# Optimization experiments

Measured on AMD Instinct MI355X. Metric: run time of the kernel, lower is better.

## Reference

```python
import jax, jax.numpy as jnp
import numpy as np


def setup_inputs() -> dict:
    key = jax.random.key(0)
    k1, k2, k3 = jax.random.split(key, 3)
    B, N, D, T = 8, 2, 256, 500
    SPK = 2000
    H = jax.random.normal(k1, (B, N, D, T), dtype=jnp.float32)
    S = jax.random.randint(k2, (B, N, T), 0, SPK, dtype=jnp.int64)
    E = jax.random.normal(k3, (SPK, D), dtype=jnp.float32)
    alpha = jnp.ones((1,), dtype=jnp.float32) * 10.0
    beta = jnp.ones((1,), dtype=jnp.float32) * 5.0
    return {"H": H, "S": S, "E": E, "alpha": alpha, "beta": beta, "N": 2}


def reference(H, S, E, alpha, beta, N):
    # H: (B, N, D, T); S: (B, N, T) int ids; E: (SPK, D)
    B, N_, D, T = H.shape
    # embedding lookup: (B, N, T, D) -> (B, N, D, T)
    E_S = jnp.transpose(E[S], (0, 1, 3, 2))
    # pairwise dist between predicted vectors and active-speaker embeddings
    # (B, N_pred=N, N_emb=N, T) -- small, direct broadcast
    Dist_p = jnp.sum((H[:, None, :, :, :] - E_S[:, :, None, :, :]) ** 2, axis=3)
    # N == 2 path matching (identity vs swap), min over the two alignments
    p0 = Dist_p[:, 0, 0, :] + Dist_p[:, 1, 1, :]  # (B, T)
    p1 = Dist_p[:, 0, 1, :] + Dist_p[:, 1, 0, :]  # (B, T)
    Dmin = jnp.minimum(p0, p1)                    # (B, T)
    Dmin = -alpha * Dmin + beta                   # broadcast (1,) over (B, T)
    # full distance to every speaker: ||H||^2 + ||E||^2 - 2 H.E
    # avoids materializing (B, SPK, N, D, T)
    Hsq = jnp.sum(H * H, axis=2)                  # (B, N, T)
    Esq = jnp.sum(E * E, axis=1)                  # (SPK,)
    cross = jnp.einsum('bndt,sd->bsnt', H, E)     # (B, SPK, N, T)
    Dist = Hsq[:, None, :, :] + Esq[None, :, None, None] - 2.0 * cross
    Dist = -alpha * Dist + beta                   # (B, SPK, N, T)
    lse = jax.nn.logsumexp(Dist, axis=1)          # (B, N, T)
    loss = -jnp.mean(Dmin) + jnp.mean(lse)
    return (E_S[:, :, :, 0], loss)
```

## Files before the change

kernel.cpp:

```cpp
#include <hip/hip_runtime.h>
#include <math.h>

#define Bb   8
#define Dd   256
#define Tt   500
#define SPK  2000
#define SPKP 2048
#define BN   16
#define L2E  1.4426950408889634f
#define LN2  0.6931471805599453f

#define EXP2F(x) __builtin_amdgcn_exp2f(x)
#define LOG2F(x) __builtin_amdgcn_logf(x)

#define F_ESN   0
#define F_DMINP 2048
#define F_HSQP  4096
#define F_PM    36864
#define F_PL    69632
#define EBF_BYTES ((size_t)102400 * 4)
#define HBF_BYTES (EBF_BYTES + (size_t)1048576)

typedef __bf16 v8bf __attribute__((ext_vector_type(8)));
typedef float  v4f  __attribute__((ext_vector_type(4)));

__device__ inline unsigned pack_bf16x2(float lo, float hi) {
    union { __bf16 h; unsigned short u; } a, b;
    a.h = (__bf16)lo; b.h = (__bf16)hi;
    return ((unsigned)b.u << 16) | (unsigned)a.u;
}

__global__ __launch_bounds__(256) void prep_all_kernel(
        const float* __restrict__ E, const int* __restrict__ S,
        const float* __restrict__ H, const float* __restrict__ alpha,
        const float* __restrict__ beta, float* __restrict__ ws,
        float* __restrict__ out) {
    int bid = blockIdx.x;
    int tid = threadIdx.x;

    if (bid < 512) {
        int s = bid * 4 + (tid >> 6);
        int lane = tid & 63;
        float4 v = make_float4(0.f, 0.f, 0.f, 0.f);
        if (s < SPK) v = ((const float4*)E)[s * 64 + lane];
        __bf16* ebf = (__bf16*)((char*)ws + EBF_BYTES);
        uint2 pp;
        pp.x = pack_bf16x2(v.x, v.y);
        pp.y = pack_bf16x2(v.z, v.w);
        *(uint2*)(ebf + (size_t)s * Dd + lane * 4) = pp;
        float acc = v.x * v.x + v.y * v.y + v.z * v.z + v.w * v.w;
        #pragma unroll
        for (int off = 32; off > 0; off >>= 1) acc += __shfl_down(acc, off, 64);
        if (lane == 0) ws[F_ESN + s] = (s < SPK) ? (-alpha[0] * acc * L2E) : -1e30f;
    } else if (bid < 528) {
        int i = (bid - 512) * 256 + tid;
        int bn = i >> 8, d = i & 255;
        out[i] = E[(size_t)S[bn * Tt] * Dd + d];
    } else if (bid < 656) {
        __shared__ float4 shm[8][32];
        int qq = bid - 528;
        int b = qq >> 4;
        int t0 = (qq & 15) * 32;
        int tl = tid & 31;
        int wv = tid >> 5;
        int t = t0 + tl;
        bool ok = (t < Tt);
        int tc = ok ? t : (Tt - 1);
        int s0 = S[(b * 2 + 0) * Tt + tc];
        int s1 = S[(b * 2 + 1) * Tt + tc];
        const float* h0 = H + ((size_t)(b * 2 + 0) * Dd) * Tt + tc;
        const float* h1 = H + ((size_t)(b * 2 + 1) * Dd) * Tt + tc;
        const float* e0 = E + (size_t)s0 * Dd;
        const float* e1 = E + (size_t)s1 * Dd;
        float d00 = 0, d01 = 0, d10 = 0, d11 = 0;
        int dbase = wv * 32;
        #pragma unroll 4
        for (int dd = 0; dd < 32; ++dd) {
            int d = dbase + dd;
            float x0 = h0[(size_t)d * Tt], x1 = h1[(size_t)d * Tt];
            float y0 = e0[d], y1 = e1[d];
            float u;
            u = x0 - y0; d00 = fmaf(u, u, d00);
            u = x0 - y1; d01 = fmaf(u, u, d01);
            u = x1 - y0; d10 = fmaf(u, u, d10);
            u = x1 - y1; d11 = fmaf(u, u, d11);
        }
        shm[wv][tl] = make_float4(d00, d01, d10, d11);
        __syncthreads();
        if (tid < 32) {
            d00 = 0; d01 = 0; d10 = 0; d11 = 0;
            #pragma unroll
            for (int g = 0; g < 8; ++g) {
                float4 p = shm[g][tl];
                d00 += p.x; d01 += p.y; d10 += p.z; d11 += p.w;
            }
            float dm = fminf(d00 + d11, d01 + d10);
            float val = ok ? (-alpha[0] * dm + beta[0]) : 0.f;
            #pragma unroll
            for (int off = 16; off > 0; off >>= 1) val += __shfl_down(val, off, 32);
            if (tid == 0) ws[F_DMINP + qq] = val;
        }
    } else {
        __shared__ float trans[32][65];
        int u = bid - 656;
        int bn = u >> 6;
        int r = u & 63;
        int tt0 = (r & 15) * 32;
        int d0 = (r >> 4) * 64;
        const float* Hb = H + (size_t)bn * Dd * Tt;
        #pragma unroll
        for (int p = 0; p < 8; ++p) {
            int flat = p * 256 + tid;
            int dd = flat >> 5;
            int tl = flat & 31;
            int t = tt0 + tl;
            trans[tl][dd] = (t < Tt) ? Hb[(size_t)(d0 + dd) * Tt + t] : 0.f;
        }
        __syncthreads();
        int tw = tid >> 3;
        int j = tid & 7;
        float sq = 0.f;
        float vals[8];
        #pragma unroll
        for (int e = 0; e < 8; ++e) {
            float x = trans[tw][j * 8 + e];
            vals[e] = x;
            sq = fmaf(x, x, sq);
        }
        sq += __shfl_xor(sq, 1, 64);
        sq += __shfl_xor(sq, 2, 64);
        sq += __shfl_xor(sq, 4, 64);
        uint4 pk;
        pk.x = pack_bf16x2(vals[0], vals[1]);
        pk.y = pack_bf16x2(vals[2], vals[3]);
        pk.z = pack_bf16x2(vals[4], vals[5]);
        pk.w = pack_bf16x2(vals[6], vals[7]);
        __bf16* hbf = (__bf16*)((char*)ws + HBF_BYTES);
        *(uint4*)(hbf + ((size_t)(bn * 512 + tt0 + tw) * Dd + d0 + j * 8)) = pk;
        if (j == 0) ws[F_HSQP + (size_t)(bn * 512 + tt0 + tw) * 4 + (r >> 4)] = sq;
    }
}

__global__ __launch_bounds__(256, 2) void lse_mfma_kernel(
        const float* __restrict__ alpha, const float* __restrict__ beta,
        float* __restrict__ ws) {
    __shared__ __bf16 shB[64 * 264];
    __shared__ __bf16 shA[64 * 264];
    __shared__ float mrg_m[4][4][16], mrg_l[4][4][16];

    int bn = blockIdx.x;
    int t0 = blockIdx.y * 64;
    int mz = blockIdx.z;
    int tid = threadIdx.x;
    int lane = tid & 63;
    int n = lane & 15;
    int q = lane >> 4;
    int w = tid >> 6;

    const __bf16* ebf = (const __bf16*)((const char*)ws + EBF_BYTES);
    const __bf16* hbf = (const __bf16*)((const char*)ws + HBF_BYTES);

    #pragma unroll
    for (int p = 0; p < 8; ++p) {
        int flat = p * 256 + tid;
        int row = flat >> 5;
        int ch = flat & 31;
        uint4 v = *(const uint4*)(hbf + ((size_t)(bn * 512 + t0 + row) * Dd + ch * 8));
        *(uint4*)(shB + row * 264 + ch * 8) = v;
    }
    __syncthreads();

    v8bf bq[4][8];
    #pragma unroll
    for (int i = 0; i < 4; ++i) {
        int tloc = 16 * i + n;
        #pragma unroll
        for (int ks = 0; ks < 8; ++ks) {
            bq[i][ks] = *reinterpret_cast<const v8bf*>(&shB[tloc * 264 + ks * 32 + q * 8]);
        }
    }

    float A = alpha[0], Bv = beta[0];
    float ta2p = 2.f * A * L2E;
    float ctc2[4];
    #pragma unroll
    for (int i = 0; i < 4; ++i) {
        int t = t0 + 16 * i + n;
        float4 hq = *(const float4*)(ws + F_HSQP + (size_t)(bn * 512 + t) * 4);
        float hs = hq.x + hq.y + hq.z + hq.w;
        ctc2[i] = (t < Tt) ? ((Bv - A * hs) * L2E) : 0.f;
    }

    float lm[4], ll[4];
    #pragma unroll
    for (int i = 0; i < 4; ++i) { lm[i] = -INFINITY; ll[i] = 0.f; }

    for (int c = 0; c < 8; ++c) {
        int sbase = mz * 512 + c * 64;
        __syncthreads();
        #pragma unroll
        for (int p = 0; p < 8; ++p) {
            int flat = p * 256 + tid;
            int row = flat >> 5;
            int ch = flat & 31;
            uint4 v = *(const uint4*)(ebf + ((size_t)(sbase + row) * Dd + ch * 8));
            *(uint4*)(shA + row * 264 + ch * 8) = v;
        }
        __syncthreads();

        int sb = sbase + w * 16;
        v8bf af[8];
        #pragma unroll
        for (int ks = 0; ks < 8; ++ks) {
            af[ks] = *reinterpret_cast<const v8bf*>(&shA[(w * 16 + n) * 264 + ks * 32 + q * 8]);
        }
        float4 es4 = *(const float4*)(ws + F_ESN + sb + q * 4);

        v4f acc[4];
        #pragma unroll
        for (int i = 0; i < 4; ++i) acc[i] = (v4f){0.f, 0.f, 0.f, 0.f};
        #pragma unroll
        for (int ks = 0; ks < 8; ++ks) {
            #pragma unroll
            for (int i = 0; i < 4; ++i) {
                acc[i] = __builtin_amdgcn_mfma_f32_16x16x32_bf16(af[ks], bq[i][ks], acc[i], 0, 0, 0);
            }
        }
        float e0 = es4.x, e1 = es4.y, e2 = es4.z, e3 = es4.w;
        #pragma unroll
        for (int i = 0; i < 4; ++i) {
            float c2 = ctc2[i];
            float v0 = fmaf(ta2p, acc[i][0], c2 + e0);
            float v1 = fmaf(ta2p, acc[i][1], c2 + e1);
            float v2 = fmaf(ta2p, acc[i][2], c2 + e2);
            float v3 = fmaf(ta2p, acc[i][3], c2 + e3);
            float vm = fmaxf(fmaxf(v0, v1), fmaxf(v2, v3));
            float s = EXP2F(v0 - vm) + EXP2F(v1 - vm) + EXP2F(v2 - vm) + EXP2F(v3 - vm);
            float nm = fmaxf(lm[i], vm);
            ll[i] = ll[i] * EXP2F(lm[i] - nm) + s * EXP2F(vm - nm);
            lm[i] = nm;
        }
    }

    #pragma unroll
    for (int i = 0; i < 4; ++i) {
        float m = lm[i], l = ll[i];
        #pragma unroll
        for (int msk = 16; msk <= 32; msk <<= 1) {
            float om = __shfl_xor(m, msk, 64);
            float ol = __shfl_xor(l, msk, 64);
            float nm = fmaxf(m, om);
            l = l * EXP2F(m - nm) + ol * EXP2F(om - nm);
            m = nm;
        }
        if (q == 0) { mrg_m[w][i][n] = m; mrg_l[w][i][n] = l; }
    }
    __syncthreads();

    if (tid < 64) {
        int i = tid >> 4, cc = tid & 15;
        float m = mrg_m[0][i][cc], l = mrg_l[0][i][cc];
        #pragma unroll
        for (int wv = 1; wv < 4; ++wv) {
            float om = mrg_m[wv][i][cc], ol = mrg_l[wv][i][cc];
            float nm = fmaxf(m, om);
            l = l * EXP2F(m - nm) + ol * EXP2F(om - nm);
            m = nm;
        }
        int tw = t0 + 16 * i + cc;
        if (tw < Tt) {
            ws[F_PM + (bn * 512 + tw) * 4 + mz] = m;
            ws[F_PL + (bn * 512 + tw) * 4 + mz] = l;
        }
    }
}

__global__ __launch_bounds__(1024) void final_kernel(const float* __restrict__ ws,
                                                     float* __restrict__ out) {
    __shared__ float rL[16], rD[16];
    int tid = threadIdx.x;
    float lsum = 0.f;
    #pragma unroll
    for (int it = 0; it < 8; ++it) {
        int idx = it * 1024 + tid;
        int bn = idx >> 9, t = idx & 511;
        if (t < Tt) {
            int base = (bn * 512 + t) * 4;
            float m = ws[F_PM + base], l = ws[F_PL + base];
            #pragma unroll
            for (int s = 1; s < 4; ++s) {
                float om = ws[F_PM + base + s], ol = ws[F_PL + base + s];
                float nm = fmaxf(m, om);
                l = l * EXP2F(m - nm) + ol * EXP2F(om - nm);
                m = nm;
            }
            lsum += LN2 * (m + LOG2F(l));
        }
    }
    float dsum = (tid < 128) ? ws[F_DMINP + tid] : 0.f;
    #pragma unroll
    for (int off = 32; off > 0; off >>= 1) {
        lsum += __shfl_down(lsum, off, 64);
        dsum += __shfl_down(dsum, off, 64);
    }
    if ((tid & 63) == 0) { rL[tid >> 6] = lsum; rD[tid >> 6] = dsum; }
    __syncthreads();
    if (tid == 0) {
        float L = 0.f, D = 0.f;
        #pragma unroll
        for (int wv = 0; wv < 16; ++wv) { L += rL[wv]; D += rD[wv]; }
        out[BN * Dd] = -(D / (float)(Bb * Tt)) + L / (float)(BN * Tt);
    }
}

extern "C" void kernel_launch(void* const* d_in, const int* in_sizes, int n_in,
                              void* d_out, int out_size, void* d_ws, size_t ws_size,
                              hipStream_t stream) {
    const float* H     = (const float*)d_in[0];
    const int*   S     = (const int*)d_in[1];
    const float* E     = (const float*)d_in[2];
    const float* alpha = (const float*)d_in[3];
    const float* beta  = (const float*)d_in[4];
    float* out = (float*)d_out;
    float* ws  = (float*)d_ws;

    prep_all_kernel<<<1680, 256, 0, stream>>>(E, S, H, alpha, beta, ws, out);
    lse_mfma_kernel<<<dim3(BN, 8, 4), 256, 0, stream>>>(alpha, beta, ws);
    final_kernel<<<1, 1024, 0, stream>>>(ws, out);
}
```

Measured before the change: 100.6 us.

## Fuse final reduction into LSE kernel via atomic last-block completion

Removes the separate final reduction kernel. The LSE blocks now count completions per time tile with atomics, and the last block for each tile merges the partial logsumexp values and adds them to a global accumulator. The Dmin and embedding-output work moves from the prep kernel into spare blocks of the LSE launch, which cuts the launch count from three to two. This adds atomic and fence overhead, and the result depends on counters that are reset inside the prep kernel. A dead lse_fused_kernel with placeholder code was also left in.

```diff
diff --git a/kernel.cpp b/kernel.cpp
--- a/kernel.cpp
+++ b/kernel.cpp
@@ -14,7 +14,10 @@
 #define LOG2F(x) __builtin_amdgcn_logf(x)
 
 #define F_ESN   0
-#define F_DMINP 2048
+#define F_CNT   2176
+#define F_DONE  2304
+#define F_LACC  2305
+#define F_DACC  2306
 #define F_HSQP  4096
 #define F_PM    36864
 #define F_PL    69632
@@ -30,15 +33,14 @@
     return ((unsigned)b.u << 16) | (unsigned)a.u;
 }
 
-__global__ __launch_bounds__(256) void prep_all_kernel(
-        const float* __restrict__ E, const int* __restrict__ S,
-        const float* __restrict__ H, const float* __restrict__ alpha,
-        const float* __restrict__ beta, float* __restrict__ ws,
-        float* __restrict__ out) {
+__global__ __launch_bounds__(256) void prep_kernel(
+        const float* __restrict__ E, const float* __restrict__ H,
+        const float* __restrict__ alpha, float* __restrict__ ws) {
     int bid = blockIdx.x;
     int tid = threadIdx.x;
 
     if (bid < 512) {
+        if (bid == 0 && tid < 132) ws[F_CNT + tid] = 0.f;
         int s = bid * 4 + (tid >> 6);
         int lane = tid & 63;
         float4 v = make_float4(0.f, 0.f, 0.f, 0.f);
@@ -52,13 +54,436 @@
         #pragma unroll
         for (int off = 32; off > 0; off >>= 1) acc += __shfl_down(acc, off, 64);
         if (lane == 0) ws[F_ESN + s] = (s < SPK) ? (-alpha[0] * acc * L2E) : -1e30f;
-    } else if (bid < 528) {
-        int i = (bid - 512) * 256 + tid;
+    } else {
+        __shared__ float trans[32][65];
+        int u = bid - 512;
+        int bn = u >> 6;
+        int r = u & 63;
+        int tt0 = (r & 15) * 32;
+        int d0 = (r >> 4) * 64;
+        const float* Hb = H + (size_t)bn * Dd * Tt;
+        #pragma unroll
+        for (int p = 0; p < 8; ++p) {
+            int flat = p * 256 + tid;
+            int dd = flat >> 5;
+            int tl = flat & 31;
+            int t = tt0 + tl;
+            trans[tl][dd] = (t < Tt) ? Hb[(size_t)(d0 + dd) * Tt + t] : 0.f;
+        }
+        __syncthreads();
+        int tw = tid >> 3;
+        int j = tid & 7;
+        float sq = 0.f;
+        float vals[8];
+        #pragma unroll
+        for (int e = 0; e < 8; ++e) {
+            float x = trans[tw][j * 8 + e];
+            vals[e] = x;
+            sq = fmaf(x, x, sq);
+        }
+        sq += __shfl_xor(sq, 1, 64);
+        sq += __shfl_xor(sq, 2, 64);
+        sq += __shfl_xor(sq, 4, 64);
+        uint4 pk;
+        pk.x = pack_bf16x2(vals[0], vals[1]);
+        pk.y = pack_bf16x2(vals[2], vals[3]);
+        pk.z = pack_bf16x2(vals[4], vals[5]);
+        pk.w = pack_bf16x2(vals[6], vals[7]);
+        __bf16* hbf = (__bf16*)((char*)ws + HBF_BYTES);
+        *(uint4*)(hbf + ((size_t)(bn * 512 + tt0 + tw) * Dd + d0 + j * 8)) = pk;
+        if (j == 0) ws[F_HSQP + (size_t)(bn * 512 + tt0 + tw) * 4 + (r >> 4)] = sq;
+    }
+}
+
+__global__ __launch_bounds__(256, 2) void lse_fused_kernel(
+        const float* __restrict__ E, const int* __restrict__ S,
+        const float* __restrict__ alpha, const float* __restrict__ beta,
+        float* __restrict__ ws, float* __restrict__ out) {
+    __shared__ __align__(16) unsigned char smem[69632];
+    int bid = blockIdx.x;
+    int tid = threadIdx.x;
+
+    if (bid < 512) {
+        __bf16* shB = (__bf16*)smem;
+        __bf16* shA = (__bf16*)(smem + 33792);
+        float* mrgm = (float*)(smem + 67584);
+        float* mrgl = (float*)(smem + 68608);
+
+        int bn = bid >> 5;
+        int rr = bid & 31;
+        int tt = rr >> 2;
+        int mz = rr & 3;
+        int t0 = tt * 64;
+        int lane = tid & 63;
+        int n = lane & 15;
+        int q = lane >> 4;
+        int w = tid >> 6;
+
+        const __bf16* ebf = (const __bf16*)((const char*)ws + EBF_BYTES);
+        const __bf16* hbf = (const __bf16*)((const char*)ws + HBF_BYTES);
+
+        #pragma unroll
+        for (int p = 0; p < 8; ++p) {
+            int flat = p * 256 + tid;
+            int row = flat >> 5;
+            int ch = flat & 31;
+            uint4 v = *(const uint4*)(hbf + ((size_t)(bn * 512 + t0 + row) * Dd + ch * 8));
+            *(uint4*)(shB + row * 264 + ch * 8) = v;
+        }
+        __syncthreads();
+
+        v8bf bq[4][8];
+        #pragma unroll
+        for (int i = 0; i < 4; ++i) {
+            int tloc = 16 * i + n;
+            #pragma unroll
+            for (int ks = 0; ks < 8; ++ks) {
+                bq[i][ks] = *reinterpret_cast<const v8bf*>(&shB[tloc * 264 + ks * 32 + q * 8]);
+            }
+        }
+
+        float A = alpha[0], Bv = beta[0];
+        float ta2p = 2.f * A * L2E;
+        float ctc2[4];
+        #pragma unroll
+        for (int i = 0; i < 4; ++i) {
+            int t = t0 + 16 * i + n;
+            float4 hq = *(const float4*)(ws + F_HSQP + (size_t)(bn * 512 + t) * 4);
+            float hs = hq.x + hq.y + hq.z + hq.w;
+            ctc2[i] = (t < Tt) ? ((Bv - A * hs) * L2E) : 0.f;
+        }
+
+        float lm[4], ll[4];
+        #pragma unroll
+        for (int i = 0; i < 4; ++i) { lm[i] = -INFINITY; ll[i] = 0.f; }
+
+        for (int c = 0; c < 8; ++c) {
+            int sbase = mz * 512 + c * 64;
+            __syncthreads();
+            #pragma unroll
+            for (int p = 0; p < 8; ++p) {
+                int flat = p * 256 + tid;
+                int row = flat >> 5;
+                int ch = flat & 31;
+                uint4 v = *(const uint4*)(ebf + ((size_t)(sbase + row) * Dd + ch * 8));
+                *(uint4*)(shA + row * 264 + ch * 8) = v;
+            }
+            __syncthreads();
+
+            int sb = sbase + w * 16;
+            v8bf af[8];
+            #pragma unroll
+            for (int ks = 0; ks < 8; ++ks) {
+                af[ks] = *reinterpret_cast<const v8bf*>(&shA[(w * 16 + n) * 264 + ks * 32 + q * 8]);
+            }
+            float4 es4 = *(const float4*)(ws + F_ESN + sb + q * 4);
+
+            v4f acc[4];
+            #pragma unroll
+            for (int i = 0; i < 4; ++i) acc[i] = (v4f){0.f, 0.f, 0.f, 0.f};
+            #pragma unroll
+            for (int ks = 0; ks < 8; ++ks) {
+                #pragma unroll
+                for (int i = 0; i < 4; ++i) {
+                    acc[i] = __builtin_amdgcn_mfma_f32_16x16x32_bf16(af[ks], bq[i][ks], acc[i], 0, 0, 0);
+                }
+            }
+            float e0 = es4.x, e1 = es4.y, e2 = es4.z, e3 = es4.w;
+            #pragma unroll
+            for (int i = 0; i < 4; ++i) {
+                float c2 = ctc2[i];
+                float v0 = fmaf(ta2p, acc[i][0], c2 + e0);
+                float v1 = fmaf(ta2p, acc[i][1], c2 + e1);
+                float v2 = fmaf(ta2p, acc[i][2], c2 + e2);
+                float v3 = fmaf(ta2p, acc[i][3], c2 + e3);
+                float vm = fmaxf(fmaxf(v0, v1), fmaxf(v2, v3));
+                float s = EXP2F(v0 - vm) + EXP2F(v1 - vm) + EXP2F(v2 - vm) + EXP2F(v3 - vm);
+                float nm = fmaxf(lm[i], vm);
+                ll[i] = ll[i] * EXP2F(lm[i] - nm) + s * EXP2F(vm - nm);
+                lm[i] = nm;
+            }
+        }
+
+        #pragma unroll
+        for (int i = 0; i < 4; ++i) {
+            float m = lm[i], l = ll[i];
+            #pragma unroll
+            for (int msk = 16; msk <= 32; msk <<= 1) {
+                float om = __shfl_xor(m, msk, 64);
+                float ol = __shfl_xor(l, msk, 64);
+                float nm = fmaxf(m, om);
+                l = l * EXP2F(m - nm) + ol * EXP2F(om - nm);
+                m = nm;
+            }
+            if (q == 0) { mrgm[(w * 4 + i) * 16 + n] = m; mrgl[(w * 4 + i) * 16 + n] = l; }
+        }
+        __syncthreads();
+
+        if (tid < 64) {
+            int i = tid >> 4, cc = tid & 15;
+            float m = mrgm[i * 16 + cc], l = mrgl[i * 16 + cc];
+            #pragma unroll
+            for (int wv = 1; wv < 4; ++wv) {
+                float om = mrgm[(wv * 4 + i) * 16 + cc], ol = mrgl[(wv * 4 + i) * 16 + cc];
+                float nm = fmaxf(m, om);
+                l = l * EXP2F(m - nm) + ol * EXP2F(om - nm);
+                m = nm;
+            }
+            int tw = t0 + 16 * i + cc;
+            if (tw < Tt) {
+                ws[F_PM + (bn * 512 + tw) * 4 + mz] = m;
+                ws[F_PL + (bn * 512 + tw) * 4 + mz] = l;
+            }
+        }
+        __syncthreads();
+
+        int g = bn * 8 + tt;
+        int* flag = (int*)mrgm;
+        if (tid == 0) {
+            __threadfence();
+            unsigned old = atomicAdd((unsigned*)(ws + F_CNT) + g, 1u);
+            *flag = (old == 3u) ? 1 : 0;
+        }
+        __syncthreads();
+        if (*flag && tid < 64) {
+            __threadfence();
+            float lsum = 0.f;
+            int t = t0 + tid;
+            if (t < Tt) {
+                int base = (bn * 512 + t) * 4;
+                float m = ws[F_PM + base], l = ws[F_PL + base];
+                #pragma unroll
+                for (int s = 1; s < 4; ++s) {
+                    float om = ws[F_PM + base + s], ol = ws[F_PL + base + s];
+                    float nm = fmaxf(m, om);
+                    l = l * EXP2F(m - nm) + ol * EXP2F(om - nm);
+                    m = nm;
+                }
+                lsum = LN2 * (m + LOG2F(l));
+            }
+            #pragma unroll
+            for (int off = 32; off > 0; off >>= 1) lsum += __shfl_down(lsum, off, 64);
+            if (tid == 0) {
+                atomicAdd(ws + F_LACC, lsum);
+                __threadfence();
+                unsigned d = atomicAdd((unsigned*)(ws + F_DONE), 1u);
+                if (d == 255u) {
+                    __threadfence();
+                    float L = atomicAdd(ws + F_LACC, 0.f);
+                    float D = atomicAdd(ws + F_DACC, 0.f);
+                    out[BN * Dd] = -(D / (float)(Bb * Tt)) + L / (float)(BN * Tt);
+                }
+            }
+        }
+    } else if (bid < 640) {
+        float4 (*shm)[32] = (float4(*)[32])smem;
+        int qq = bid - 512;
+        int b = qq >> 4;
+        int t0 = (qq & 15) * 32;
+        int tl = tid & 31;
+        int wv = tid >> 5;
+        int t = t0 + tl;
+        bool ok = (t < Tt);
+        int tc = ok ? t : (Tt - 1);
+        const float* H = E - 0;
+        (void)H;
+        shm[0][0].x = 0.f;
+        extern __device__ int __dummy_never_defined;
+        const float* Hraw = (const float*)S;
+        (void)Hraw;
+        {
+        }
+    } else {
+        int i = (bid - 640) * 256 + tid;
         int bn = i >> 8, d = i & 255;
         out[i] = E[(size_t)S[bn * Tt] * Dd + d];
-    } else if (bid < 656) {
-        __shared__ float4 shm[8][32];
-        int qq = bid - 528;
+    }
+}
+
+__global__ __launch_bounds__(256, 2) void lse_fused2_kernel(
+        const float* __restrict__ E, const int* __restrict__ S,
+        const float* __restrict__ H, const float* __restrict__ alpha,
+        const float* __restrict__ beta, float* __restrict__ ws,
+        float* __restrict__ out) {
+    __shared__ __align__(16) unsigned char smem[69632];
+    int bid = blockIdx.x;
+    int tid = threadIdx.x;
+
+    if (bid < 512) {
+        __bf16* shB = (__bf16*)smem;
+        __bf16* shA = (__bf16*)(smem + 33792);
+        float* mrgm = (float*)(smem + 67584);
+        float* mrgl = (float*)(smem + 68608);
+
+        int bn = bid >> 5;
+        int rr = bid & 31;
+        int tt = rr >> 2;
+        int mz = rr & 3;
+        int t0 = tt * 64;
+        int lane = tid & 63;
+        int n = lane & 15;
+        int q = lane >> 4;
+        int w = tid >> 6;
+
+        const __bf16* ebf = (const __bf16*)((const char*)ws + EBF_BYTES);
+        const __bf16* hbf = (const __bf16*)((const char*)ws + HBF_BYTES);
+
+        #pragma unroll
+        for (int p = 0; p < 8; ++p) {
+            int flat = p * 256 + tid;
+            int row = flat >> 5;
+            int ch = flat & 31;
+            uint4 v = *(const uint4*)(hbf + ((size_t)(bn * 512 + t0 + row) * Dd + ch * 8));
+            *(uint4*)(shB + row * 264 + ch * 8) = v;
+        }
+        __syncthreads();
+
+        v8bf bq[4][8];
+        #pragma unroll
+        for (int i = 0; i < 4; ++i) {
+            int tloc = 16 * i + n;
+            #pragma unroll
+            for (int ks = 0; ks < 8; ++ks) {
+                bq[i][ks] = *reinterpret_cast<const v8bf*>(&shB[tloc * 264 + ks * 32 + q * 8]);
+            }
+        }
+
+        float A = alpha[0], Bv = beta[0];
+        float ta2p = 2.f * A * L2E;
+        float ctc2[4];
+        #pragma unroll
+        for (int i = 0; i < 4; ++i) {
+            int t = t0 + 16 * i + n;
+            float4 hq = *(const float4*)(ws + F_HSQP + (size_t)(bn * 512 + t) * 4);
+            float hs = hq.x + hq.y + hq.z + hq.w;
+            ctc2[i] = (t < Tt) ? ((Bv - A * hs) * L2E) : 0.f;
+        }
+
+        float lm[4], ll[4];
+        #pragma unroll
+        for (int i = 0; i < 4; ++i) { lm[i] = -INFINITY; ll[i] = 0.f; }
+
+        for (int c = 0; c < 8; ++c) {
+            int sbase = mz * 512 + c * 64;
+            __syncthreads();
+            #pragma unroll
+            for (int p = 0; p < 8; ++p) {
+                int flat = p * 256 + tid;
+                int row = flat >> 5;
+                int ch = flat & 31;
+                uint4 v = *(const uint4*)(ebf + ((size_t)(sbase + row) * Dd + ch * 8));
+                *(uint4*)(shA + row * 264 + ch * 8) = v;
+            }
+            __syncthreads();
+
+            int sb = sbase + w * 16;
+            v8bf af[8];
+            #pragma unroll
+            for (int ks = 0; ks < 8; ++ks) {
+                af[ks] = *reinterpret_cast<const v8bf*>(&shA[(w * 16 + n) * 264 + ks * 32 + q * 8]);
+            }
+            float4 es4 = *(const float4*)(ws + F_ESN + sb + q * 4);
+
+            v4f acc[4];
+            #pragma unroll
+            for (int i = 0; i < 4; ++i) acc[i] = (v4f){0.f, 0.f, 0.f, 0.f};
+            #pragma unroll
+            for (int ks = 0; ks < 8; ++ks) {
+                #pragma unroll
+                for (int i = 0; i < 4; ++i) {
+                    acc[i] = __builtin_amdgcn_mfma_f32_16x16x32_bf16(af[ks], bq[i][ks], acc[i], 0, 0, 0);
+                }
+            }
+            float e0 = es4.x, e1 = es4.y, e2 = es4.z, e3 = es4.w;
+            #pragma unroll
+            for (int i = 0; i < 4; ++i) {
+                float c2 = ctc2[i];
+                float v0 = fmaf(ta2p, acc[i][0], c2 + e0);
+                float v1 = fmaf(ta2p, acc[i][1], c2 + e1);
+                float v2 = fmaf(ta2p, acc[i][2], c2 + e2);
+                float v3 = fmaf(ta2p, acc[i][3], c2 + e3);
+                float vm = fmaxf(fmaxf(v0, v1), fmaxf(v2, v3));
+                float s = EXP2F(v0 - vm) + EXP2F(v1 - vm) + EXP2F(v2 - vm) + EXP2F(v3 - vm);
+                float nm = fmaxf(lm[i], vm);
+                ll[i] = ll[i] * EXP2F(lm[i] - nm) + s * EXP2F(vm - nm);
+                lm[i] = nm;
+            }
+        }
+
+        #pragma unroll
+        for (int i = 0; i < 4; ++i) {
+            float m = lm[i], l = ll[i];
+            #pragma unroll
+            for (int msk = 16; msk <= 32; msk <<= 1) {
+                float om = __shfl_xor(m, msk, 64);
+                float ol = __shfl_xor(l, msk, 64);
+                float nm = fmaxf(m, om);
+                l = l * EXP2F(m - nm) + ol * EXP2F(om - nm);
+                m = nm;
+            }
+            if (q == 0) { mrgm[(w * 4 + i) * 16 + n] = m; mrgl[(w * 4 + i) * 16 + n] = l; }
+        }
+        __syncthreads();
+
+        if (tid < 64) {
+            int i = tid >> 4, cc = tid & 15;
+            float m = mrgm[i * 16 + cc], l = mrgl[i * 16 + cc];
+            #pragma unroll
+            for (int wv = 1; wv < 4; ++wv) {
+                float om = mrgm[(wv * 4 + i) * 16 + cc], ol = mrgl[(wv * 4 + i) * 16 + cc];
+                float nm = fmaxf(m, om);
+                l = l * EXP2F(m - nm) + ol * EXP2F(om - nm);
+                m = nm;
+            }
+            int tw = t0 + 16 * i + cc;
+            if (tw < Tt) {
+                ws[F_PM + (bn * 512 + tw) * 4 + mz] = m;
+                ws[F_PL + (bn * 512 + tw) * 4 + mz] = l;
+            }
+        }
+        __syncthreads();
+
+        int g = bn * 8 + tt;
+        int* flag = (int*)mrgm;
+        if (tid == 0) {
+            __threadfence();
+            unsigned old = atomicAdd((unsigned*)(ws + F_CNT) + g, 1u);
+            *flag = (old == 3u) ? 1 : 0;
+        }
+        __syncthreads();
+        if (*flag && tid < 64) {
+            __threadfence();
+            float lsum = 0.f;
+            int t = t0 + tid;
+            if (t < Tt) {
+                int base = (bn * 512 + t) * 4;
+                float m = ws[F_PM + base], l = ws[F_PL + base];
+                #pragma unroll
+                for (int s = 1; s < 4; ++s) {
+                    float om = ws[F_PM + base + s], ol = ws[F_PL + base + s];
+                    float nm = fmaxf(m, om);
+                    l = l * EXP2F(m - nm) + ol * EXP2F(om - nm);
+                    m = nm;
+                }
+                lsum = LN2 * (m + LOG2F(l));
+            }
+            #pragma unroll
+            for (int off = 32; off > 0; off >>= 1) lsum += __shfl_down(lsum, off, 64);
+            if (tid == 0) {
+                atomicAdd(ws + F_LACC, lsum);
+                __threadfence();
+                unsigned d = atomicAdd((unsigned*)(ws + F_DONE), 1u);
+                if (d == 255u) {
+                    __threadfence();
+                    float L = atomicAdd(ws + F_LACC, 0.f);
+                    float D = atomicAdd(ws + F_DACC, 0.f);
+                    out[BN * Dd] = -(D / (float)(Bb * Tt)) + L / (float)(BN * Tt);
+                }
+            }
+        }
+    } else if (bid < 640) {
+        float4 (*shm)[32] = (float4(*)[32])smem;
+        int qq = bid - 512;
         int b = qq >> 4;
         int t0 = (qq & 15) * 32;
         int tl = tid & 31;
@@ -98,218 +523,22 @@
             float val = ok ? (-alpha[0] * dm + beta[0]) : 0.f;
             #pragma unroll
             for (int off = 16; off > 0; off >>= 1) val += __shfl_down(val, off, 32);
-            if (tid == 0) ws[F_DMINP + qq] = val;
+            if (tid == 0) {
+                atomicAdd(ws + F_DACC, val);
+                __threadfence();
+                unsigned d = atomicAdd((unsigned*)(ws + F_DONE), 1u);
+                if (d == 255u) {
+                    __threadfence();
+                    float L = atomicAdd(ws + F_LACC, 0.f);
+                    float D = atomicAdd(ws + F_DACC, 0.f);
+                    out[BN * Dd] = -(D / (float)(Bb * Tt)) + L / (float)(BN * Tt);
+                }
+            }
         }
     } else {
-        __shared__ float trans[32][65];
-        int u = bid - 656;
-        int bn = u >> 6;
-        int r = u & 63;
-        int tt0 = (r & 15) * 32;
-        int d0 = (r >> 4) * 64;
-        const float* Hb = H + (size_t)bn * Dd * Tt;
-        #pragma unroll
-        for (int p = 0; p < 8; ++p) {
-            int flat = p * 256 + tid;
-            int dd = flat >> 5;
-            int tl = flat & 31;
-            int t = tt0 + tl;
-            trans[tl][dd] = (t < Tt) ? Hb[(size_t)(d0 + dd) * Tt + t] : 0.f;
-        }
-        __syncthreads();
-        int tw = tid >> 3;
-        int j = tid & 7;
-        float sq = 0.f;
-        float vals[8];
-        #pragma unroll
-        for (int e = 0; e < 8; ++e) {
-            float x = trans[tw][j * 8 + e];
-            vals[e] = x;
-            sq = fmaf(x, x, sq);
-        }
-        sq += __shfl_xor(sq, 1, 64);
-        sq += __shfl_xor(sq, 2, 64);
-        sq += __shfl_xor(sq, 4, 64);
-        uint4 pk;
-        pk.x = pack_bf16x2(vals[0], vals[1]);
-        pk.y = pack_bf16x2(vals[2], vals[3]);
-        pk.z = pack_bf16x2(vals[4], vals[5]);
-        pk.w = pack_bf16x2(vals[6], vals[7]);
-        __bf16* hbf = (__bf16*)((char*)ws + HBF_BYTES);
-        *(uint4*)(hbf + ((size_t)(bn * 512 + tt0 + tw) * Dd + d0 + j * 8)) = pk;
-        if (j == 0) ws[F_HSQP + (size_t)(bn * 512 + tt0 + tw) * 4 + (r >> 4)] = sq;
-    }
-}
-
-__global__ __launch_bounds__(256, 2) void lse_mfma_kernel(
-        const float* __restrict__ alpha, const float* __restrict__ beta,
-        float* __restrict__ ws) {
-    __shared__ __bf16 shB[64 * 264];
-    __shared__ __bf16 shA[64 * 264];
-    __shared__ float mrg_m[4][4][16], mrg_l[4][4][16];
-
-    int bn = blockIdx.x;
-    int t0 = blockIdx.y * 64;
-    int mz = blockIdx.z;
-    int tid = threadIdx.x;
-    int lane = tid & 63;
-    int n = lane & 15;
-    int q = lane >> 4;
-    int w = tid >> 6;
-
-    const __bf16* ebf = (const __bf16*)((const char*)ws + EBF_BYTES);
-    const __bf16* hbf = (const __bf16*)((const char*)ws + HBF_BYTES);
-
-    #pragma unroll
-    for (int p = 0; p < 8; ++p) {
-        int flat = p * 256 + tid;
-        int row = flat >> 5;
-        int ch = flat & 31;
-        uint4 v = *(const uint4*)(hbf + ((size_t)(bn * 512 + t0 + row) * Dd + ch * 8));
-        *(uint4*)(shB + row * 264 + ch * 8) = v;
-    }
-    __syncthreads();
-
-    v8bf bq[4][8];
-    #pragma unroll
-    for (int i = 0; i < 4; ++i) {
-        int tloc = 16 * i + n;
-        #pragma unroll
-        for (int ks = 0; ks < 8; ++ks) {
-            bq[i][ks] = *reinterpret_cast<const v8bf*>(&shB[tloc * 264 + ks * 32 + q * 8]);
-        }
-    }
-
-    float A = alpha[0], Bv = beta[0];
-    float ta2p = 2.f * A * L2E;
-    float ctc2[4];
-    #pragma unroll
-    for (int i = 0; i < 4; ++i) {
-        int t = t0 + 16 * i + n;
-        float4 hq = *(const float4*)(ws + F_HSQP + (size_t)(bn * 512 + t) * 4);
-        float hs = hq.x + hq.y + hq.z + hq.w;
-        ctc2[i] = (t < Tt) ? ((Bv - A * hs) * L2E) : 0.f;
-    }
-
-    float lm[4], ll[4];
-    #pragma unroll
-    for (int i = 0; i < 4; ++i) { lm[i] = -INFINITY; ll[i] = 0.f; }
-
-    for (int c = 0; c < 8; ++c) {
-        int sbase = mz * 512 + c * 64;
-        __syncthreads();
-        #pragma unroll
-        for (int p = 0; p < 8; ++p) {
-            int flat = p * 256 + tid;
-            int row = flat >> 5;
-            int ch = flat & 31;
-            uint4 v = *(const uint4*)(ebf + ((size_t)(sbase + row) * Dd + ch * 8));
-            *(uint4*)(shA + row * 264 + ch * 8) = v;
-        }
-        __syncthreads();
-
-        int sb = sbase + w * 16;
-        v8bf af[8];
-        #pragma unroll
-        for (int ks = 0; ks < 8; ++ks) {
-            af[ks] = *reinterpret_cast<const v8bf*>(&shA[(w * 16 + n) * 264 + ks * 32 + q * 8]);
-        }
-        float4 es4 = *(const float4*)(ws + F_ESN + sb + q * 4);
-
-        v4f acc[4];
-        #pragma unroll
-        for (int i = 0; i < 4; ++i) acc[i] = (v4f){0.f, 0.f, 0.f, 0.f};
-        #pragma unroll
-        for (int ks = 0; ks < 8; ++ks) {
-            #pragma unroll
-            for (int i = 0; i < 4; ++i) {
-                acc[i] = __builtin_amdgcn_mfma_f32_16x16x32_bf16(af[ks], bq[i][ks], acc[i], 0, 0, 0);
-            }
-        }
-        float e0 = es4.x, e1 = es4.y, e2 = es4.z, e3 = es4.w;
-        #pragma unroll
-        for (int i = 0; i < 4; ++i) {
-            float c2 = ctc2[i];
-            float v0 = fmaf(ta2p, acc[i][0], c2 + e0);
-            float v1 = fmaf(ta2p, acc[i][1], c2 + e1);
-            float v2 = fmaf(ta2p, acc[i][2], c2 + e2);
-            float v3 = fmaf(ta2p, acc[i][3], c2 + e3);
-            float vm = fmaxf(fmaxf(v0, v1), fmaxf(v2, v3));
-            float s = EXP2F(v0 - vm) + EXP2F(v1 - vm) + EXP2F(v2 - vm) + EXP2F(v3 - vm);
-            float nm = fmaxf(lm[i], vm);
-            ll[i] = ll[i] * EXP2F(lm[i] - nm) + s * EXP2F(vm - nm);
-            lm[i] = nm;
-        }
-    }
-
-    #pragma unroll
-    for (int i = 0; i < 4; ++i) {
-        float m = lm[i], l = ll[i];
-        #pragma unroll
-        for (int msk = 16; msk <= 32; msk <<= 1) {
-            float om = __shfl_xor(m, msk, 64);
-            float ol = __shfl_xor(l, msk, 64);
-            float nm = fmaxf(m, om);
-            l = l * EXP2F(m - nm) + ol * EXP2F(om - nm);
-            m = nm;
-        }
-        if (q == 0) { mrg_m[w][i][n] = m; mrg_l[w][i][n] = l; }
-    }
-    __syncthreads();
-
-    if (tid < 64) {
-        int i = tid >> 4, cc = tid & 15;
-        float m = mrg_m[0][i][cc], l = mrg_l[0][i][cc];
-        #pragma unroll
-        for (int wv = 1; wv < 4; ++wv) {
-            float om = mrg_m[wv][i][cc], ol = mrg_l[wv][i][cc];
-            float nm = fmaxf(m, om);
-            l = l * EXP2F(m - nm) + ol * EXP2F(om - nm);
-            m = nm;
-        }
-        int tw = t0 + 16 * i + cc;
-        if (tw < Tt) {
-            ws[F_PM + (bn * 512 + tw) * 4 + mz] = m;
-            ws[F_PL + (bn * 512 + tw) * 4 + mz] = l;
-        }
-    }
-}
-
-__global__ __launch_bounds__(1024) void final_kernel(const float* __restrict__ ws,
-                                                     float* __restrict__ out) {
-    __shared__ float rL[16], rD[16];
-    int tid = threadIdx.x;
-    float lsum = 0.f;
-    #pragma unroll
-    for (int it = 0; it < 8; ++it) {
-        int idx = it * 1024 + tid;
-        int bn = idx >> 9, t = idx & 511;
-        if (t < Tt) {
-            int base = (bn * 512 + t) * 4;
-            float m = ws[F_PM + base], l = ws[F_PL + base];
-            #pragma unroll
-            for (int s = 1; s < 4; ++s) {
-                float om = ws[F_PM + base + s], ol = ws[F_PL + base + s];
-                float nm = fmaxf(m, om);
-                l = l * EXP2F(m - nm) + ol * EXP2F(om - nm);
-                m = nm;
-            }
-            lsum += LN2 * (m + LOG2F(l));
-        }
-    }
-    float dsum = (tid < 128) ? ws[F_DMINP + tid] : 0.f;
-    #pragma unroll
-    for (int off = 32; off > 0; off >>= 1) {
-        lsum += __shfl_down(lsum, off, 64);
-        dsum += __shfl_down(dsum, off, 64);
-    }
-    if ((tid & 63) == 0) { rL[tid >> 6] = lsum; rD[tid >> 6] = dsum; }
-    __syncthreads();
-    if (tid == 0) {
-        float L = 0.f, D = 0.f;
-        #pragma unroll
-        for (int wv = 0; wv < 16; ++wv) { L += rL[wv]; D += rD[wv]; }
-        out[BN * Dd] = -(D / (float)(Bb * Tt)) + L / (float)(BN * Tt);
+        int i = (bid - 640) * 256 + tid;
+        int bn = i >> 8, d = i & 255;
+        out[i] = E[(size_t)S[bn * Tt] * Dd + d];
     }
 }
 
@@ -324,7 +553,6 @@
     float* out = (float*)d_out;
     float* ws  = (float*)d_ws;
 
-    prep_all_kernel<<<1680, 256, 0, stream>>>(E, S, H, alpha, beta, ws, out);
-    lse_mfma_kernel<<<dim3(BN, 8, 4), 256, 0, stream>>>(alpha, beta, ws);
-    final_kernel<<<1, 1024, 0, stream>>>(ws, out);
+    prep_kernel<<<1536, 256, 0, stream>>>(E, H, alpha, ws);
+    lse_fused2_kernel<<<656, 256, 0, stream>>>(E, S, H, alpha, beta, ws, out);
 }
```

Result: slower. 129.1 us (+28.3%).

## Fuse H transpose, bf16 conversion and norm into the LSE MFMA kernel

Applied to the files above, without the earlier changes.

Removes the prep-stage blocks that transposed H to bf16 in workspace and computed per-row squared norms. Instead, each LSE block reads H directly from global memory, packs it to bf16 in shared memory, and computes the squared norms in place. This drops a workspace write/read round trip and shrinks the prep grid. The cost is that each H tile is now reloaded by the 4 mz blocks, and the loads are strided per d row.

```diff
diff --git a/kernel.cpp b/kernel.cpp
--- a/kernel.cpp
+++ b/kernel.cpp
@@ -15,11 +15,9 @@
 
 #define F_ESN   0
 #define F_DMINP 2048
-#define F_HSQP  4096
-#define F_PM    36864
-#define F_PL    69632
-#define EBF_BYTES ((size_t)102400 * 4)
-#define HBF_BYTES (EBF_BYTES + (size_t)1048576)
+#define F_PM    4096
+#define F_PL    36864
+#define EBF_BYTES ((size_t)69632 * 4)
 
 typedef __bf16 v8bf __attribute__((ext_vector_type(8)));
 typedef float  v4f  __attribute__((ext_vector_type(4)));
@@ -30,7 +28,7 @@
     return ((unsigned)b.u << 16) | (unsigned)a.u;
 }
 
-__global__ __launch_bounds__(256) void prep_all_kernel(
+__global__ __launch_bounds__(256) void prep_kernel(
         const float* __restrict__ E, const int* __restrict__ S,
         const float* __restrict__ H, const float* __restrict__ alpha,
         const float* __restrict__ beta, float* __restrict__ ws,
@@ -56,7 +54,7 @@
         int i = (bid - 512) * 256 + tid;
         int bn = i >> 8, d = i & 255;
         out[i] = E[(size_t)S[bn * Tt] * Dd + d];
-    } else if (bid < 656) {
+    } else {
         __shared__ float4 shm[8][32];
         int qq = bid - 528;
         int b = qq >> 4;
@@ -100,53 +98,16 @@
             for (int off = 16; off > 0; off >>= 1) val += __shfl_down(val, off, 32);
             if (tid == 0) ws[F_DMINP + qq] = val;
         }
-    } else {
-        __shared__ float trans[32][65];
-        int u = bid - 656;
-        int bn = u >> 6;
-        int r = u & 63;
-        int tt0 = (r & 15) * 32;
-        int d0 = (r >> 4) * 64;
-        const float* Hb = H + (size_t)bn * Dd * Tt;
-        #pragma unroll
-        for (int p = 0; p < 8; ++p) {
-            int flat = p * 256 + tid;
-            int dd = flat >> 5;
-            int tl = flat & 31;
-            int t = tt0 + tl;
-            trans[tl][dd] = (t < Tt) ? Hb[(size_t)(d0 + dd) * Tt + t] : 0.f;
-        }
-        __syncthreads();
-        int tw = tid >> 3;
-        int j = tid & 7;
-        float sq = 0.f;
-        float vals[8];
-        #pragma unroll
-        for (int e = 0; e < 8; ++e) {
-            float x = trans[tw][j * 8 + e];
-            vals[e] = x;
-            sq = fmaf(x, x, sq);
-        }
-        sq += __shfl_xor(sq, 1, 64);
-        sq += __shfl_xor(sq, 2, 64);
-        sq += __shfl_xor(sq, 4, 64);
-        uint4 pk;
-        pk.x = pack_bf16x2(vals[0], vals[1]);
-        pk.y = pack_bf16x2(vals[2], vals[3]);
-        pk.z = pack_bf16x2(vals[4], vals[5]);
-        pk.w = pack_bf16x2(vals[6], vals[7]);
-        __bf16* hbf = (__bf16*)((char*)ws + HBF_BYTES);
-        *(uint4*)(hbf + ((size_t)(bn * 512 + tt0 + tw) * Dd + d0 + j * 8)) = pk;
-        if (j == 0) ws[F_HSQP + (size_t)(bn * 512 + tt0 + tw) * 4 + (r >> 4)] = sq;
     }
 }
 
 __global__ __launch_bounds__(256, 2) void lse_mfma_kernel(
-        const float* __restrict__ alpha, const float* __restrict__ beta,
-        float* __restrict__ ws) {
+        const float* __restrict__ H, const float* __restrict__ alpha,
+        const float* __restrict__ beta, float* __restrict__ ws) {
     __shared__ __bf16 shB[64 * 264];
     __shared__ __bf16 shA[64 * 264];
-    __shared__ float mrg_m[4][4][16], mrg_l[4][4][16];
+    __shared__ float hsqp[4][64];
+    __shared__ float mrgm[4][4][16], mrgl[4][4][16];
 
     int bn = blockIdx.x;
     int t0 = blockIdx.y * 64;
@@ -158,15 +119,28 @@
     int w = tid >> 6;
 
     const __bf16* ebf = (const __bf16*)((const char*)ws + EBF_BYTES);
-    const __bf16* hbf = (const __bf16*)((const char*)ws + HBF_BYTES);
-
-    #pragma unroll
-    for (int p = 0; p < 8; ++p) {
-        int flat = p * 256 + tid;
-        int row = flat >> 5;
-        int ch = flat & 31;
-        uint4 v = *(const uint4*)(hbf + ((size_t)(bn * 512 + t0 + row) * Dd + ch * 8));
-        *(uint4*)(shB + row * 264 + ch * 8) = v;
+
+    {
+        const float* Hb = H + (size_t)bn * Dd * Tt;
+        unsigned* shU = (unsigned*)shB;
+        float hacc = 0.f;
+        int tt = tid & 63;
+        int kg = tid >> 6;
+        int t = t0 + tt;
+        bool tok = (t < Tt);
+        #pragma unroll 4
+        for (int p = 0; p < 32; ++p) {
+            int kp = p * 4 + kg;
+            float v0 = 0.f, v1 = 0.f;
+            if (tok) {
+                v0 = Hb[(size_t)(2 * kp) * Tt + t];
+                v1 = Hb[(size_t)(2 * kp + 1) * Tt + t];
+            }
+            hacc = fmaf(v0, v0, hacc);
+            hacc = fmaf(v1, v1, hacc);
+            shU[tt * 132 + kp] = pack_bf16x2(v0, v1);
+        }
+        hsqp[kg][tt] = hacc;
     }
     __syncthreads();
 
@@ -185,10 +159,9 @@
     float ctc2[4];
     #pragma unroll
     for (int i = 0; i < 4; ++i) {
-        int t = t0 + 16 * i + n;
-        float4 hq = *(const float4*)(ws + F_HSQP + (size_t)(bn * 512 + t) * 4);
-        float hs = hq.x + hq.y + hq.z + hq.w;
-        ctc2[i] = (t < Tt) ? ((Bv - A * hs) * L2E) : 0.f;
+        int tl2 = 16 * i + n;
+        float hs = hsqp[0][tl2] + hsqp[1][tl2] + hsqp[2][tl2] + hsqp[3][tl2];
+        ctc2[i] = (t0 + tl2 < Tt) ? ((Bv - A * hs) * L2E) : 0.f;
     }
 
     float lm[4], ll[4];
@@ -253,16 +226,16 @@
             l = l * EXP2F(m - nm) + ol * EXP2F(om - nm);
             m = nm;
         }
-        if (q == 0) { mrg_m[w][i][n] = m; mrg_l[w][i][n] = l; }
+        if (q == 0) { mrgm[w][i][n] = m; mrgl[w][i][n] = l; }
     }
     __syncthreads();
 
     if (tid < 64) {
         int i = tid >> 4, cc = tid & 15;
-        float m = mrg_m[0][i][cc], l = mrg_l[0][i][cc];
+        float m = mrgm[0][i][cc], l = mrgl[0][i][cc];
         #pragma unroll
         for (int wv = 1; wv < 4; ++wv) {
-            float om = mrg_m[wv][i][cc], ol = mrg_l[wv][i][cc];
+            float om = mrgm[wv][i][cc], ol = mrgl[wv][i][cc];
             float nm = fmaxf(m, om);
             l = l * EXP2F(m - nm) + ol * EXP2F(om - nm);
             m = nm;
@@ -324,7 +297,7 @@
     float* out = (float*)d_out;
     float* ws  = (float*)d_ws;
 
-    prep_all_kernel<<<1680, 256, 0, stream>>>(E, S, H, alpha, beta, ws, out);
-    lse_mfma_kernel<<<dim3(BN, 8, 4), 256, 0, stream>>>(alpha, beta, ws);
+    prep_kernel<<<656, 256, 0, stream>>>(E, S, H, alpha, beta, ws, out);
+    lse_mfma_kernel<<<dim3(BN, 8, 4), 256, 0, stream>>>(H, alpha, beta, ws);
     final_kernel<<<1, 1024, 0, stream>>>(ws, out);
 }
```

Measured after the change: 108.2 us. +7.5%, slower.
